# Kernel tuning notes

Hardware: AMD Instinct MI355X
Metric: run time of the kernel (lower is better)

Reference implementation:

```python
import jax, jax.numpy as jnp
import numpy as np

EPS = 1e-5


def _conv(x, k, stride, pad):
    # k: (kh, kw, Cin, Cout). Original code flattens kernel in (ki,kj,c) order
    # but the input patch in (c,ki,kj) order; reproduce that exact pairing by
    # re-flattening the kernel into (c,ki,kj,o) layout.
    kh, kw, cin, cout = k.shape
    k_eff = k.reshape(kh * kw * cin, cout).reshape(cin, kh, kw, cout)
    w = jnp.transpose(k_eff, (3, 0, 1, 2))  # OIHW
    return jax.lax.conv_general_dilated(
        x, w, window_strides=(stride, stride),
        padding=((pad, pad), (pad, pad)),
        dimension_numbers=('NCHW', 'OIHW', 'NCHW'))


def _maxpool(x, k, stride, pad):
    # Original pads with ZEROS, then takes window max.
    xp = jnp.pad(x, ((0, 0), (0, 0), (pad, pad), (pad, pad)))
    return jax.lax.reduce_window(
        xp, -jnp.inf, jax.lax.max,
        window_dimensions=(1, 1, k, k), window_strides=(1, 1, stride, stride),
        padding='VALID')


def _bn_eval(x, gamma, beta):
    # eval-mode BatchNorm with initial moving stats: mean=0, var=1
    return gamma * (x / jnp.sqrt(1.0 + EPS)) + beta


def setup_inputs() -> dict:
    key = jax.random.key(0)
    ks = jax.random.split(key, 8)
    B, H, n_cls = 512, 128, 6
    fc_in = 16 * 32 * 32  # 16 channels, 32x32 spatial after encoder for H=128

    def kaiming(k, shape, fan_in):
        bound = float(np.sqrt(6.0 / fan_in))
        return jax.random.uniform(k, shape, jnp.float32, -bound, bound)

    return {
        'x': jax.random.uniform(ks[0], (B, 3, H, H), jnp.float32),
        'k1': kaiming(ks[1], (5, 5, 3, 5), 5 * 5 * 3),
        'gamma': jnp.ones((1, 5, 1, 1), jnp.float32),
        'beta': jnp.zeros((1, 5, 1, 1), jnp.float32),
        'k2': kaiming(ks[2], (3, 3, 5, 9), 3 * 3 * 5),
        'k3': kaiming(ks[3], (3, 3, 9, 16), 3 * 3 * 9),
        'fc_w': kaiming(ks[4], (n_cls, fc_in), fc_in),
        'fc_b': jnp.zeros((n_cls,), jnp.float32),
    }


def reference(x, k1, gamma, beta, k2, k3, fc_w, fc_b):
    h = _conv(x, k1, stride=1, pad=1)          # [B,5,126,126]
    h = jax.nn.relu(h)
    h = _bn_eval(h, gamma, beta)
    h = _maxpool(h, 3, 2, 1)                   # [B,5,63,63]
    h = _conv(h, k2, stride=1, pad=1)          # [B,9,63,63]
    h = jax.nn.relu(h)
    h = _maxpool(h, 3, 2, 1)                   # [B,9,32,32]
    h = _conv(h, k3, stride=1, pad=1)          # [B,16,32,32]
    flat = h.reshape(h.shape[0], -1)           # [B,16384]
    logits = flat @ fc_w.T + fc_b              # [B,6]
    return jax.nn.softmax(logits, axis=1)
```

## Files before the change

### kernel.cpp

```cpp
#include <hip/hip_runtime.h>
#include <math.h>

__global__ __launch_bounds__(256) void conv1_pool_kernel(
    const float* __restrict__ x, const float* __restrict__ k1,
    const float* __restrict__ gamma, const float* __restrict__ beta,
    float* __restrict__ out1)
{
    const int b    = blockIdx.y;
    const int tile = blockIdx.x;
    const int ty = tile >> 2, tx = tile & 3;
    const int tid = threadIdx.x;

    __shared__ float sIn[3][37][39];

    const int iy0 = 32 * ty - 2, ix0 = 32 * tx - 2;
    for (int idx = tid; idx < 3 * 37 * 37; idx += 256) {
        int c  = idx / 1369;
        int r  = idx - c * 1369;
        int ly = r / 37, lx = r - ly * 37;
        int gy = iy0 + ly, gx = ix0 + lx;
        float v = 0.f;
        if ((unsigned)gy < 128u && (unsigned)gx < 128u)
            v = x[((b * 3 + c) * 128 + gy) * 128 + gx];
        sIn[c][ly][lx] = v;
    }
    __syncthreads();

    const int lpy = tid >> 4, lpx = tid & 15;
    const int py = 16 * ty + lpy, px = 16 * tx + lpx;
    if (py >= 63 || px >= 63) return;

    const float invs = rsqrtf(1.0f + 1e-5f);
    float sc[5], bt[5];
#pragma unroll
    for (int o = 0; o < 5; ++o) { sc[o] = gamma[o] * invs; bt[o] = beta[o]; }

    float mx[5];
#pragma unroll
    for (int o = 0; o < 5; ++o) mx[o] = -1e30f;

    for (int dy = 0; dy < 3; ++dy) {
        const int cy = 2 * py - 1 + dy;
        for (int dx = 0; dx < 3; ++dx) {
            const int cx = 2 * px - 1 + dx;
            if (cy < 0 || cx < 0) {
#pragma unroll
                for (int o = 0; o < 5; ++o) mx[o] = fmaxf(mx[o], 0.f);
                continue;
            }
            float acc[5] = {0.f, 0.f, 0.f, 0.f, 0.f};
#pragma unroll
            for (int c = 0; c < 3; ++c)
#pragma unroll
                for (int ki = 0; ki < 5; ++ki)
#pragma unroll
                    for (int kj = 0; kj < 5; ++kj) {
                        float iv = sIn[c][2 * lpy + dy + ki][2 * lpx + dx + kj];
                        const float* w = &k1[((c * 5 + ki) * 5 + kj) * 5];
#pragma unroll
                        for (int o = 0; o < 5; ++o)
                            acc[o] = fmaf(iv, w[o], acc[o]);
                    }
#pragma unroll
            for (int o = 0; o < 5; ++o) {
                float v = fmaxf(acc[o], 0.f) * sc[o] + bt[o];
                mx[o] = fmaxf(mx[o], v);
            }
        }
    }
#pragma unroll
    for (int o = 0; o < 5; ++o)
        out1[((b * 5 + o) * 63 + py) * 63 + px] = mx[o];
}

__global__ __launch_bounds__(256) void conv2_pool_kernel(
    const float* __restrict__ in1, const float* __restrict__ k2,
    float* __restrict__ out2)
{
    const int b    = blockIdx.y;
    const int tile = blockIdx.x;
    const int ty = tile >> 1, tx = tile & 1;
    const int tid = threadIdx.x;

    __shared__ float sIn[5][35][37];

    const int iy0 = 32 * ty - 2, ix0 = 32 * tx - 2;
    for (int idx = tid; idx < 5 * 35 * 35; idx += 256) {
        int c  = idx / 1225;
        int r  = idx - c * 1225;
        int ly = r / 35, lx = r - ly * 35;
        int gy = iy0 + ly, gx = ix0 + lx;
        float v = 0.f;
        if ((unsigned)gy < 63u && (unsigned)gx < 63u)
            v = in1[((b * 5 + c) * 63 + gy) * 63 + gx];
        sIn[c][ly][lx] = v;
    }
    __syncthreads();

    const int lpy = tid >> 4, lpx = tid & 15;
    const int py = 16 * ty + lpy, px = 16 * tx + lpx;

    float mx[9];
#pragma unroll
    for (int o = 0; o < 9; ++o) mx[o] = 0.f;

    for (int dy = 0; dy < 3; ++dy) {
        const int cy = 2 * py - 1 + dy;
        if (cy < 0 || cy >= 63) continue;
        for (int dx = 0; dx < 3; ++dx) {
            const int cx = 2 * px - 1 + dx;
            if (cx < 0 || cx >= 63) continue;
            float acc[9] = {0.f,0.f,0.f,0.f,0.f,0.f,0.f,0.f,0.f};
#pragma unroll
            for (int c = 0; c < 5; ++c)
#pragma unroll
                for (int ki = 0; ki < 3; ++ki)
#pragma unroll
                    for (int kj = 0; kj < 3; ++kj) {
                        float iv = sIn[c][2 * lpy + dy + ki][2 * lpx + dx + kj];
                        const float* w = &k2[((c * 3 + ki) * 3 + kj) * 9];
#pragma unroll
                        for (int o = 0; o < 9; ++o)
                            acc[o] = fmaf(iv, w[o], acc[o]);
                    }
#pragma unroll
            for (int o = 0; o < 9; ++o) mx[o] = fmaxf(mx[o], acc[o]);
        }
    }
#pragma unroll
    for (int o = 0; o < 9; ++o)
        out2[((b * 9 + o) * 32 + py) * 32 + px] = mx[o];
}

__global__ __launch_bounds__(256) void conv3_fc_kernel(
    const float* __restrict__ in2, const float* __restrict__ k3,
    const float* __restrict__ fcw, const float* __restrict__ fcb,
    float* __restrict__ out)
{
    const int b   = blockIdx.x;
    const int tid = threadIdx.x;

    __shared__ float sP[9][34][36];
    __shared__ float sRed[4][6];

    for (int idx = tid; idx < 9 * 34 * 36; idx += 256) {
        int c  = idx / (34 * 36);
        int r  = idx - c * (34 * 36);
        int yy = r / 36, xx = r - yy * 36;
        float v = 0.f;
        if (yy >= 1 && yy < 33 && xx >= 1 && xx < 33)
            v = in2[((b * 9 + c) * 32 + (yy - 1)) * 32 + (xx - 1)];
        sP[c][yy][xx] = v;
    }
    __syncthreads();

    float acc6[6] = {0.f,0.f,0.f,0.f,0.f,0.f};
    for (int j = 0; j < 4; ++j) {
        const int s = tid + 256 * j;
        const int y = s >> 5, xc = s & 31;
        float acc16[16];
#pragma unroll
        for (int o = 0; o < 16; ++o) acc16[o] = 0.f;
#pragma unroll
        for (int c = 0; c < 9; ++c) {
            float iv[9];
#pragma unroll
            for (int ki = 0; ki < 3; ++ki)
#pragma unroll
                for (int kj = 0; kj < 3; ++kj)
                    iv[ki * 3 + kj] = sP[c][y + ki][xc + kj];
#pragma unroll
            for (int ki = 0; ki < 3; ++ki)
#pragma unroll
                for (int kj = 0; kj < 3; ++kj) {
                    float v = iv[ki * 3 + kj];
                    const float* w = &k3[((c * 3 + ki) * 3 + kj) * 16];
#pragma unroll
                    for (int o = 0; o < 16; ++o)
                        acc16[o] = fmaf(v, w[o], acc16[o]);
                }
        }
#pragma unroll
        for (int o = 0; o < 16; ++o) {
            const int f = o * 1024 + s;
#pragma unroll
            for (int cls = 0; cls < 6; ++cls)
                acc6[cls] = fmaf(acc16[o], fcw[cls * 16384 + f], acc6[cls]);
        }
    }

#pragma unroll
    for (int cls = 0; cls < 6; ++cls) {
        float v = acc6[cls];
#pragma unroll
        for (int off = 32; off >= 1; off >>= 1)
            v += __shfl_xor(v, off, 64);
        if ((tid & 63) == 0) sRed[tid >> 6][cls] = v;
    }
    __syncthreads();
    if (tid == 0) {
        float logits[6], mxl = -1e30f;
        for (int cls = 0; cls < 6; ++cls) {
            float l = sRed[0][cls] + sRed[1][cls] + sRed[2][cls] + sRed[3][cls]
                      + fcb[cls];
            logits[cls] = l;
            mxl = fmaxf(mxl, l);
        }
        float ssum = 0.f;
        for (int cls = 0; cls < 6; ++cls) {
            logits[cls] = expf(logits[cls] - mxl);
            ssum += logits[cls];
        }
        for (int cls = 0; cls < 6; ++cls)
            out[b * 6 + cls] = logits[cls] / ssum;
    }
}

extern "C" void kernel_launch(void* const* d_in, const int* in_sizes, int n_in,
                              void* d_out, int out_size, void* d_ws, size_t ws_size,
                              hipStream_t stream)
{
    const float* x     = (const float*)d_in[0];
    const float* k1    = (const float*)d_in[1];
    const float* gamma = (const float*)d_in[2];
    const float* beta  = (const float*)d_in[3];
    const float* k2    = (const float*)d_in[4];
    const float* k3    = (const float*)d_in[5];
    const float* fcw   = (const float*)d_in[6];
    const float* fcb   = (const float*)d_in[7];
    float* out = (float*)d_out;

    float* out1 = (float*)d_ws;
    float* out2 = out1 + (size_t)512 * 5 * 63 * 63;

    conv1_pool_kernel<<<dim3(16, 512), 256, 0, stream>>>(x, k1, gamma, beta, out1);
    conv2_pool_kernel<<<dim3(4, 512), 256, 0, stream>>>(out1, k2, out2);
    conv3_fc_kernel<<<dim3(512), 256, 0, stream>>>(out2, k3, fcw, fcb, out);
}
```

Before: 505.9 us.

## Compute conv tiles once into shared memory before pooling, widen conv3 block

In the conv1 and conv2 pooling kernels, each thread previously recomputed the overlapping 3x3 pool-window convolutions (about 2.25x redundant work). They now compute the 33x33 conv tile once into shared memory, with each thread producing 5 adjacent outputs using register-reused input rows, then take the pool max from shared memory. The conv3+FC kernel moves to 1024 threads per block with one spatial position per thread, and the final reduction is extended to 16 waves. This adds shared-memory footprint and a second barrier, which may lower occupancy, and leaves 25 of 256 threads idle during the conv phase.

```diff
diff --git a/kernel.cpp b/kernel.cpp
--- a/kernel.cpp
+++ b/kernel.cpp
@@ -11,7 +11,8 @@
     const int ty = tile >> 2, tx = tile & 3;
     const int tid = threadIdx.x;
 
-    __shared__ float sIn[3][37][39];
+    __shared__ float sIn[3][37][40];
+    __shared__ float sConv[5][33][34];
 
     const int iy0 = 32 * ty - 2, ix0 = 32 * tx - 2;
     for (int idx = tid; idx < 3 * 37 * 37; idx += 256) {
@@ -26,51 +27,74 @@
     }
     __syncthreads();
 
+    if (tid < 231) {
+        const int ly  = tid / 7;
+        const int cg  = tid - 7 * ly;
+        const int lx0 = 5 * cg;
+        const int cy  = 32 * ty - 1 + ly;
+        const int cx0 = 32 * tx - 1 + lx0;
+
+        float acc[5][5];
+#pragma unroll
+        for (int p = 0; p < 5; ++p)
+#pragma unroll
+            for (int o = 0; o < 5; ++o) acc[p][o] = 0.f;
+
+#pragma unroll
+        for (int c = 0; c < 3; ++c)
+#pragma unroll
+            for (int ki = 0; ki < 5; ++ki) {
+                float iv[9];
+#pragma unroll
+                for (int j = 0; j < 9; ++j) iv[j] = sIn[c][ly + ki][lx0 + j];
+#pragma unroll
+                for (int kj = 0; kj < 5; ++kj) {
+                    const float* w = &k1[((c * 5 + ki) * 5 + kj) * 5];
+#pragma unroll
+                    for (int p = 0; p < 5; ++p) {
+                        float v = iv[p + kj];
+#pragma unroll
+                        for (int o = 0; o < 5; ++o)
+                            acc[p][o] = fmaf(v, w[o], acc[p][o]);
+                    }
+                }
+            }
+
+        const float invs = rsqrtf(1.0f + 1e-5f);
+        float sc[5], bt[5];
+#pragma unroll
+        for (int o = 0; o < 5; ++o) { sc[o] = gamma[o] * invs; bt[o] = beta[o]; }
+
+        const bool rowok = (unsigned)cy < 126u;
+#pragma unroll
+        for (int p = 0; p < 5; ++p) {
+            const int lx = lx0 + p;
+            if (lx < 33) {
+                const bool ok = rowok && ((unsigned)(cx0 + p) < 126u);
+#pragma unroll
+                for (int o = 0; o < 5; ++o) {
+                    float v = fmaxf(acc[p][o], 0.f) * sc[o] + bt[o];
+                    sConv[o][ly][lx] = ok ? v : 0.f;
+                }
+            }
+        }
+    }
+    __syncthreads();
+
     const int lpy = tid >> 4, lpx = tid & 15;
     const int py = 16 * ty + lpy, px = 16 * tx + lpx;
-    if (py >= 63 || px >= 63) return;
-
-    const float invs = rsqrtf(1.0f + 1e-5f);
-    float sc[5], bt[5];
-#pragma unroll
-    for (int o = 0; o < 5; ++o) { sc[o] = gamma[o] * invs; bt[o] = beta[o]; }
-
-    float mx[5];
-#pragma unroll
-    for (int o = 0; o < 5; ++o) mx[o] = -1e30f;
-
-    for (int dy = 0; dy < 3; ++dy) {
-        const int cy = 2 * py - 1 + dy;
-        for (int dx = 0; dx < 3; ++dx) {
-            const int cx = 2 * px - 1 + dx;
-            if (cy < 0 || cx < 0) {
-#pragma unroll
-                for (int o = 0; o < 5; ++o) mx[o] = fmaxf(mx[o], 0.f);
-                continue;
-            }
-            float acc[5] = {0.f, 0.f, 0.f, 0.f, 0.f};
-#pragma unroll
-            for (int c = 0; c < 3; ++c)
-#pragma unroll
-                for (int ki = 0; ki < 5; ++ki)
-#pragma unroll
-                    for (int kj = 0; kj < 5; ++kj) {
-                        float iv = sIn[c][2 * lpy + dy + ki][2 * lpx + dx + kj];
-                        const float* w = &k1[((c * 5 + ki) * 5 + kj) * 5];
-#pragma unroll
-                        for (int o = 0; o < 5; ++o)
-                            acc[o] = fmaf(iv, w[o], acc[o]);
-                    }
-#pragma unroll
-            for (int o = 0; o < 5; ++o) {
-                float v = fmaxf(acc[o], 0.f) * sc[o] + bt[o];
-                mx[o] = fmaxf(mx[o], v);
-            }
-        }
-    }
-#pragma unroll
-    for (int o = 0; o < 5; ++o)
-        out1[((b * 5 + o) * 63 + py) * 63 + px] = mx[o];
+    if (py < 63 && px < 63) {
+#pragma unroll
+        for (int o = 0; o < 5; ++o) {
+            float m = -3.4e38f;
+#pragma unroll
+            for (int dy = 0; dy < 3; ++dy)
+#pragma unroll
+                for (int dx = 0; dx < 3; ++dx)
+                    m = fmaxf(m, sConv[o][2 * lpy + dy][2 * lpx + dx]);
+            out1[((b * 5 + o) * 63 + py) * 63 + px] = m;
+        }
+    }
 }
 
 __global__ __launch_bounds__(256) void conv2_pool_kernel(
@@ -82,7 +106,8 @@
     const int ty = tile >> 1, tx = tile & 1;
     const int tid = threadIdx.x;
 
-    __shared__ float sIn[5][35][37];
+    __shared__ float sIn[5][35][38];
+    __shared__ float sConv[9][33][34];
 
     const int iy0 = 32 * ty - 2, ix0 = 32 * tx - 2;
     for (int idx = tid; idx < 5 * 35 * 35; idx += 256) {
@@ -97,42 +122,68 @@
     }
     __syncthreads();
 
+    if (tid < 231) {
+        const int ly  = tid / 7;
+        const int cg  = tid - 7 * ly;
+        const int lx0 = 5 * cg;
+        const int cy  = 32 * ty - 1 + ly;
+        const int cx0 = 32 * tx - 1 + lx0;
+
+        float acc[5][9];
+#pragma unroll
+        for (int p = 0; p < 5; ++p)
+#pragma unroll
+            for (int o = 0; o < 9; ++o) acc[p][o] = 0.f;
+
+#pragma unroll
+        for (int c = 0; c < 5; ++c)
+#pragma unroll
+            for (int ki = 0; ki < 3; ++ki) {
+                float iv[7];
+#pragma unroll
+                for (int j = 0; j < 7; ++j) iv[j] = sIn[c][ly + ki][lx0 + j];
+#pragma unroll
+                for (int kj = 0; kj < 3; ++kj) {
+                    const float* w = &k2[((c * 3 + ki) * 3 + kj) * 9];
+#pragma unroll
+                    for (int p = 0; p < 5; ++p) {
+                        float v = iv[p + kj];
+#pragma unroll
+                        for (int o = 0; o < 9; ++o)
+                            acc[p][o] = fmaf(v, w[o], acc[p][o]);
+                    }
+                }
+            }
+
+        const bool rowok = (unsigned)cy < 63u;
+#pragma unroll
+        for (int p = 0; p < 5; ++p) {
+            const int lx = lx0 + p;
+            if (lx < 33) {
+                const bool ok = rowok && ((unsigned)(cx0 + p) < 63u);
+#pragma unroll
+                for (int o = 0; o < 9; ++o)
+                    sConv[o][ly][lx] = ok ? fmaxf(acc[p][o], 0.f) : 0.f;
+            }
+        }
+    }
+    __syncthreads();
+
     const int lpy = tid >> 4, lpx = tid & 15;
     const int py = 16 * ty + lpy, px = 16 * tx + lpx;
-
-    float mx[9];
-#pragma unroll
-    for (int o = 0; o < 9; ++o) mx[o] = 0.f;
-
-    for (int dy = 0; dy < 3; ++dy) {
-        const int cy = 2 * py - 1 + dy;
-        if (cy < 0 || cy >= 63) continue;
-        for (int dx = 0; dx < 3; ++dx) {
-            const int cx = 2 * px - 1 + dx;
-            if (cx < 0 || cx >= 63) continue;
-            float acc[9] = {0.f,0.f,0.f,0.f,0.f,0.f,0.f,0.f,0.f};
-#pragma unroll
-            for (int c = 0; c < 5; ++c)
-#pragma unroll
-                for (int ki = 0; ki < 3; ++ki)
-#pragma unroll
-                    for (int kj = 0; kj < 3; ++kj) {
-                        float iv = sIn[c][2 * lpy + dy + ki][2 * lpx + dx + kj];
-                        const float* w = &k2[((c * 3 + ki) * 3 + kj) * 9];
-#pragma unroll
-                        for (int o = 0; o < 9; ++o)
-                            acc[o] = fmaf(iv, w[o], acc[o]);
-                    }
-#pragma unroll
-            for (int o = 0; o < 9; ++o) mx[o] = fmaxf(mx[o], acc[o]);
-        }
-    }
-#pragma unroll
-    for (int o = 0; o < 9; ++o)
-        out2[((b * 9 + o) * 32 + py) * 32 + px] = mx[o];
-}
-
-__global__ __launch_bounds__(256) void conv3_fc_kernel(
+#pragma unroll
+    for (int o = 0; o < 9; ++o) {
+        float m = 0.f;
+#pragma unroll
+        for (int dy = 0; dy < 3; ++dy)
+#pragma unroll
+            for (int dx = 0; dx < 3; ++dx)
+                m = fmaxf(m, sConv[o][2 * lpy + dy][2 * lpx + dx]);
+        out2[((b * 9 + o) * 32 + py) * 32 + px] = m;
+    }
+}
+
+__global__ __launch_bounds__(1024) void conv3_fc_kernel(
     const float* __restrict__ in2, const float* __restrict__ k3,
     const float* __restrict__ fcw, const float* __restrict__ fcb,
     float* __restrict__ out)
@@ -141,9 +192,9 @@
     const int tid = threadIdx.x;
 
     __shared__ float sP[9][34][36];
-    __shared__ float sRed[4][6];
-
-    for (int idx = tid; idx < 9 * 34 * 36; idx += 256) {
+    __shared__ float sRed[16][6];
+
+    for (int idx = tid; idx < 9 * 34 * 36; idx += 1024) {
         int c  = idx / (34 * 36);
         int r  = idx - c * (34 * 36);
         int yy = r / 36, xx = r - yy * 36;
@@ -154,39 +205,37 @@
     }
     __syncthreads();
 
-    float acc6[6] = {0.f,0.f,0.f,0.f,0.f,0.f};
-    for (int j = 0; j < 4; ++j) {
-        const int s = tid + 256 * j;
-        const int y = s >> 5, xc = s & 31;
-        float acc16[16];
-#pragma unroll
-        for (int o = 0; o < 16; ++o) acc16[o] = 0.f;
-#pragma unroll
-        for (int c = 0; c < 9; ++c) {
-            float iv[9];
-#pragma unroll
-            for (int ki = 0; ki < 3; ++ki)
-#pragma unroll
-                for (int kj = 0; kj < 3; ++kj)
-                    iv[ki * 3 + kj] = sP[c][y + ki][xc + kj];
-#pragma unroll
-            for (int ki = 0; ki < 3; ++ki)
-#pragma unroll
-                for (int kj = 0; kj < 3; ++kj) {
-                    float v = iv[ki * 3 + kj];
-                    const float* w = &k3[((c * 3 + ki) * 3 + kj) * 16];
-#pragma unroll
-                    for (int o = 0; o < 16; ++o)
-                        acc16[o] = fmaf(v, w[o], acc16[o]);
-                }
-        }
-#pragma unroll
-        for (int o = 0; o < 16; ++o) {
-            const int f = o * 1024 + s;
-#pragma unroll
-            for (int cls = 0; cls < 6; ++cls)
-                acc6[cls] = fmaf(acc16[o], fcw[cls * 16384 + f], acc6[cls]);
-        }
+    const int s = tid;
+    const int y = s >> 5, xc = s & 31;
+
+    float acc16[16];
+#pragma unroll
+    for (int o = 0; o < 16; ++o) acc16[o] = 0.f;
+
+#pragma unroll
+    for (int c = 0; c < 9; ++c)
+#pragma unroll
+        for (int ki = 0; ki < 3; ++ki) {
+            float iv[3];
+#pragma unroll
+            for (int j = 0; j < 3; ++j) iv[j] = sP[c][y + ki][xc + j];
+#pragma unroll
+            for (int kj = 0; kj < 3; ++kj) {
+                float v = iv[kj];
+                const float* w = &k3[((c * 3 + ki) * 3 + kj) * 16];
+#pragma unroll
+                for (int o = 0; o < 16; ++o)
+                    acc16[o] = fmaf(v, w[o], acc16[o]);
+            }
+        }
+
+    float acc6[6] = {0.f, 0.f, 0.f, 0.f, 0.f, 0.f};
+#pragma unroll
+    for (int o = 0; o < 16; ++o) {
+        const int f = o * 1024 + s;
+#pragma unroll
+        for (int cls = 0; cls < 6; ++cls)
+            acc6[cls] = fmaf(acc16[o], fcw[cls * 16384 + f], acc6[cls]);
     }
 
 #pragma unroll
@@ -199,18 +248,21 @@
     }
     __syncthreads();
     if (tid == 0) {
-        float logits[6], mxl = -1e30f;
+        float logits[6], mxl = -3.4e38f;
+#pragma unroll
         for (int cls = 0; cls < 6; ++cls) {
-            float l = sRed[0][cls] + sRed[1][cls] + sRed[2][cls] + sRed[3][cls]
-                      + fcb[cls];
+            float l = fcb[cls];
+            for (int wv = 0; wv < 16; ++wv) l += sRed[wv][cls];
             logits[cls] = l;
             mxl = fmaxf(mxl, l);
         }
         float ssum = 0.f;
+#pragma unroll
         for (int cls = 0; cls < 6; ++cls) {
             logits[cls] = expf(logits[cls] - mxl);
             ssum += logits[cls];
         }
+#pragma unroll
         for (int cls = 0; cls < 6; ++cls)
             out[b * 6 + cls] = logits[cls] / ssum;
     }
@@ -235,5 +287,5 @@
 
     conv1_pool_kernel<<<dim3(16, 512), 256, 0, stream>>>(x, k1, gamma, beta, out1);
     conv2_pool_kernel<<<dim3(4, 512), 256, 0, stream>>>(out1, k2, out2);
-    conv3_fc_kernel<<<dim3(512), 256, 0, stream>>>(out2, k3, fcw, fcb, out);
-}
+    conv3_fc_kernel<<<dim3(512), 1024, 0, stream>>>(out2, k3, fcw, fcb, out);
+}
```

After: 718.6 us. +42.0%, slower.
